# Kernel optimization log

Measured on AMD Instinct MI355X. Metric: run time of the kernel, lower is better.

## Reference

```python
import jax, jax.numpy as jnp
import numpy as np

NUM_HEADS = 4
GROUPS = 8
EPS = 1e-5


def group_norm(x, w, b):
    B, C, H, W, D = x.shape
    xg = x.reshape(B, GROUPS, C // GROUPS, H, W, D)
    mu = xg.mean(axis=(2, 3, 4, 5), keepdims=True)
    var = xg.var(axis=(2, 3, 4, 5), keepdims=True)
    xn = ((xg - mu) * jax.lax.rsqrt(var + EPS)).reshape(B, C, H, W, D)
    return xn * w[None, :, None, None, None] + b[None, :, None, None, None]


def avg_pool2x(t, H, W, D):
    # t: [N, d, H, W, D] -> [N, d, H/2, W/2, D/2] via 2x2x2 block mean
    N, d = t.shape[:2]
    t = t.reshape(N, d, H // 2, 2, W // 2, 2, D // 2, 2)
    return t.mean(axis=(3, 5, 7))


def setup_inputs() -> dict:
    key = jax.random.key(0)
    ks = jax.random.split(key, 4)
    B, C, H, W, D = 2, 128, 24, 24, 24
    x = jax.random.normal(ks[0], (B, C, H, W, D), dtype=jnp.float32)
    gn_w = jnp.ones((C,), jnp.float32)
    gn_b = jnp.zeros((C,), jnp.float32)
    qkv_w = jax.random.normal(ks[1], (3 * C, C), dtype=jnp.float32) * 0.02
    qkv_b = jnp.zeros((3 * C,), jnp.float32)
    proj_w = jax.random.normal(ks[2], (C, C), dtype=jnp.float32) * 0.02
    proj_b = jnp.zeros((C,), jnp.float32)
    return {"x": x, "gn_w": gn_w, "gn_b": gn_b, "qkv_w": qkv_w,
            "qkv_b": qkv_b, "proj_w": proj_w, "proj_b": proj_b}


def reference(x, gn_w, gn_b, qkv_w, qkv_b, proj_w, proj_b):
    B, C, H, W, D = x.shape
    hd = C // NUM_HEADS
    spatial = H * W * D
    residual = x

    xn = group_norm(x, gn_w, gn_b)
    # 1x1x1 conv == channel matmul
    qkv = jnp.einsum('oc,bchwd->bohwd', qkv_w, xn) + qkv_b[None, :, None, None, None]
    qkv = qkv.reshape(B, 3, NUM_HEADS, hd, spatial)
    q, k, v = qkv[:, 0], qkv[:, 1], qkv[:, 2]  # [B, h, d, N]

    if spatial > 1024:
        k3 = k.reshape(B * NUM_HEADS, hd, H, W, D)
        v3 = v.reshape(B * NUM_HEADS, hd, H, W, D)
        k = avg_pool2x(k3, H, W, D).reshape(B, NUM_HEADS, hd, -1)
        v = avg_pool2x(v3, H, W, D).reshape(B, NUM_HEADS, hd, -1)

    scale = hd ** -0.5
    attn = jnp.einsum('bhdn,bhdm->bhnm', q * scale, k)
    attn = jax.nn.softmax(attn, axis=-1)
    out = jnp.einsum('bhnm,bhdm->bhdn', attn, v)
    out = out.reshape(B, C, H, W, D)
    out = jnp.einsum('oc,bchwd->bohwd', proj_w, out) + proj_b[None, :, None, None, None]
    return out + residual
```

## Files before the change

### kernel.cpp

```cpp
#include <hip/hip_runtime.h>
#include <hip/hip_bf16.h>

#define SB 2
#define SC 128
#define SS 13824
#define SNH 4
#define SHD 32
#define SKV 1728
#define GN_N 221184.0f
#define QSCALE 0.25504771249f

typedef unsigned int uint;
typedef unsigned short ushort;
typedef __bf16 bf16x8 __attribute__((ext_vector_type(8)));
typedef float f32x16 __attribute__((ext_vector_type(16)));

__device__ inline ushort f2bf(float v){
  __hip_bfloat16 h = __float2bfloat16(v);
  return *reinterpret_cast<ushort*>(&h);
}
__device__ inline float bf2f(ushort u){
  union { ushort s[2]; float f; } x; x.s[0] = 0; x.s[1] = u; return x.f;
}
__device__ inline uint pk2(float a, float b){
  __hip_bfloat162 h = __float22bfloat162_rn(make_float2(a, b));
  return *reinterpret_cast<uint*>(&h);
}
__device__ inline bf16x8 ldg8(const ushort* p){
  union { uint4 q; bf16x8 b; } u;
  u.q = *reinterpret_cast<const uint4*>(p);
  return u.b;
}
__device__ inline f32x16 mfma32(bf16x8 a, bf16x8 b, f32x16 c){
  return __builtin_amdgcn_mfma_f32_32x32x16_bf16(a, b, c, 0, 0, 0);
}
__device__ inline int rowmap(int r, int hl){
  return (r & 3) + 8 * ((r >> 2) & 1) + 4 * hl + 16 * (r >> 3);
}
__device__ inline float vexp2(float x){
  float r;
  asm("v_exp_f32 %0, %1" : "=v"(r) : "v"(x));
  return r;
}

__global__ __launch_bounds__(256) void k_stats(const float* __restrict__ x, float* __restrict__ chsums){
  int bid = blockIdx.x;
  int b = bid >> 7, c = bid & 127;
  const float4* p = reinterpret_cast<const float4*>(x + (size_t)(b * 128 + c) * SS);
  float s = 0.f, q = 0.f;
  for (int i = threadIdx.x; i < SS / 4; i += 256){
    float4 v = p[i];
    s += v.x + v.y + v.z + v.w;
    q += v.x * v.x + v.y * v.y + v.z * v.z + v.w * v.w;
  }
  for (int off = 32; off; off >>= 1){ s += __shfl_down(s, off, 64); q += __shfl_down(q, off, 64); }
  __shared__ float ls[4][2];
  int w = threadIdx.x >> 6, lane = threadIdx.x & 63;
  if (lane == 0){ ls[w][0] = s; ls[w][1] = q; }
  __syncthreads();
  if (threadIdx.x == 0){
    float S = ls[0][0] + ls[1][0] + ls[2][0] + ls[3][0];
    float Q = ls[0][1] + ls[1][1] + ls[2][1] + ls[3][1];
    chsums[(b * 128 + c) * 2] = S;
    chsums[(b * 128 + c) * 2 + 1] = Q;
  }
}

__global__ __launch_bounds__(256) void k_params(const float* __restrict__ chsums,
                                                const float* __restrict__ gn_w, const float* __restrict__ gn_b,
                                                const float* __restrict__ qkv_w, const float* __restrict__ qkv_b,
                                                const float* __restrict__ proj_w,
                                                ushort* __restrict__ Wp, float* __restrict__ biasP,
                                                ushort* __restrict__ pw){
  int tid = blockIdx.x * 256 + threadIdx.x;
  if (tid < 768){
    int b = tid / 384, o = tid % 384;
    float mul = (o < 128) ? QSCALE : 1.0f;
    ushort* wrow = Wp + (size_t)(b * 384 + o) * 128;
    float acc = 0.f;
    for (int g = 0; g < 8; ++g){
      float S = 0.f, Q = 0.f;
      for (int ch = g * 16; ch < g * 16 + 16; ++ch){
        S += chsums[(b * 128 + ch) * 2];
        Q += chsums[(b * 128 + ch) * 2 + 1];
      }
      float mu = S * (1.0f / GN_N);
      float var = Q * (1.0f / GN_N) - mu * mu;
      float rs = rsqrtf(var + 1e-5f);
      for (int ci = 0; ci < 16; ++ci){
        int c = g * 16 + ci;
        float a = gn_w[c] * rs;
        float be = gn_b[c] - mu * a;
        float wv = qkv_w[o * 128 + c];
        acc += wv * be;
        wrow[c] = f2bf(wv * a * mul);
      }
    }
    biasP[b * 384 + o] = (qkv_b[o] + acc) * mul;
  } else if (tid < 896){
    int o = tid - 768;
    for (int c = 0; c < 128; ++c) pw[o * 128 + c] = f2bf(proj_w[o * 128 + c]);
  }
}

__global__ __launch_bounds__(128) void k_qkv(const float* __restrict__ x, const ushort* __restrict__ Wp,
                                             const float* __restrict__ biasP,
                                             ushort* __restrict__ Qt, ushort* __restrict__ KVt){
  int bid = blockIdx.x;
  int st2 = bid % 432;
  int b  = bid / 432;
  int t = threadIdx.x, w = t >> 6, lane = t & 63, hl = lane >> 5, ln = lane & 31;
  int s0 = st2 * 32;
  int s = s0 + ln;
  const float* xb = x + (size_t)b * 128 * SS;
  bf16x8 afr[8];
  #pragma unroll
  for (int ks = 0; ks < 8; ++ks){
    int cb = ks * 16 + hl * 8;
    float xv[8];
    #pragma unroll
    for (int j = 0; j < 8; ++j)
      xv[j] = xb[(size_t)(cb + j) * SS + s];
    union { uint u[4]; bf16x8 b8; } f;
    #pragma unroll
    for (int j2 = 0; j2 < 4; ++j2) f.u[j2] = pk2(xv[2 * j2], xv[2 * j2 + 1]);
    afr[ks] = f.b8;
  }
  for (int oi = 0; oi < 6; ++oi){
    int o0 = (w * 6 + oi) * 32;
    f32x16 acc = {};
    const ushort* wrow = Wp + (size_t)(b * 384 + o0 + ln) * 128 + hl * 8;
    #pragma unroll
    for (int ks = 0; ks < 8; ++ks)
      acc = mfma32(afr[ks], ldg8(wrow + ks * 16), acc);
    float bo = biasP[b * 384 + o0 + ln];
    if (o0 < 128){
      #pragma unroll
      for (int r = 0; r < 16; r += 2){
        int srow = s0 + rowmap(r, hl);
        uint pr = pk2(acc[r] + bo, acc[r + 1] + bo);
        Qt[(size_t)(b * SS + srow) * 128 + o0 + ln] = (ushort)pr;
        Qt[(size_t)(b * SS + srow + 1) * 128 + o0 + ln] = (ushort)(pr >> 16);
      }
    } else {
      #pragma unroll
      for (int r = 0; r < 16; r += 2){
        int srow = s0 + rowmap(r, hl);
        uint pr = pk2(acc[r] + bo, acc[r + 1] + bo);
        KVt[(size_t)(b * SS + srow) * 256 + (o0 - 128) + ln] = (ushort)pr;
        KVt[(size_t)(b * SS + srow + 1) * 256 + (o0 - 128) + ln] = (ushort)(pr >> 16);
      }
    }
  }
}

__global__ __launch_bounds__(256) void k_pool(const ushort* __restrict__ KVt,
                                              ushort* __restrict__ kfr, ushort* __restrict__ vfr){
  int bid = blockIdx.x;
  int mt = bid % 27;
  int h  = (bid / 27) & 3;
  int b  = bid / 108;
  int m0 = mt * 64;
  int t = threadIdx.x;
  int kl = t & 63, o = t >> 6;
  int m = m0 + kl;
  int h2 = m / 144; int rem = m - h2 * 144; int w2 = rem / 12; int d2 = rem - w2 * 12;
  int sb = h2 * 1152 + w2 * 48 + d2 * 2;
  const ushort* base = KVt + (size_t)b * SS * 256 + h * 32 + o * 8;
  float ks[8] = {0,0,0,0,0,0,0,0}, vs[8] = {0,0,0,0,0,0,0,0};
  #pragma unroll
  for (int i = 0; i < 2; ++i)
    #pragma unroll
    for (int jj = 0; jj < 2; ++jj)
      #pragma unroll
      for (int kk = 0; kk < 2; ++kk){
        const ushort* row = base + (size_t)(sb + i * 576 + jj * 24 + kk) * 256;
        union { uint4 q; ushort us[8]; } K8, V8;
        K8.q = *reinterpret_cast<const uint4*>(row);
        V8.q = *reinterpret_cast<const uint4*>(row + 128);
        #pragma unroll
        for (int j = 0; j < 8; ++j){ ks[j] += bf2f(K8.us[j]); vs[j] += bf2f(V8.us[j]); }
      }
  union { uint u[4]; uint4 q; } KW;
  #pragma unroll
  for (int j2 = 0; j2 < 4; ++j2)
    KW.u[j2] = pk2(ks[2 * j2] * 0.125f, ks[2 * j2 + 1] * 0.125f);
  int call = 2 * (kl >> 5) + (o >> 1);
  int lane = (kl & 31) + 32 * (o & 1);
  size_t kb_ = ((size_t)((b * 4 + h) * 27 + mt) * 4 + call) * 512 + lane * 8;
  *reinterpret_cast<uint4*>(&kfr[kb_]) = KW.q;
  __shared__ ushort V_lds[32][72];
  #pragma unroll
  for (int j2 = 0; j2 < 4; ++j2){
    uint pv = pk2(vs[2 * j2] * 0.125f, vs[2 * j2 + 1] * 0.125f);
    V_lds[o * 8 + 2 * j2][kl] = (ushort)pv;
    V_lds[o * 8 + 2 * j2 + 1][kl] = (ushort)(pv >> 16);
  }
  __syncthreads();
  int d = t & 31, ko = t >> 5;
  uint4 vv = *reinterpret_cast<const uint4*>(&V_lds[d][ko * 8]);
  int c = ko >> 1, hl2 = ko & 1;
  int lane2 = d + 32 * hl2;
  size_t vb_ = ((size_t)((b * 4 + h) * 27 + mt) * 4 + c) * 512 + lane2 * 8;
  *reinterpret_cast<uint4*>(&vfr[vb_]) = vv;
}

#define PVSTEP(Parr, i4, vf, oac)                                    \
  {                                                                  \
    uint a0 = Parr[(i4) + 0], a1 = Parr[(i4) + 1];                   \
    uint b0 = Parr[(i4) + 2], b1 = Parr[(i4) + 3];                   \
    asm("v_permlane32_swap_b32 %0, %1" : "+v"(a0), "+v"(b0));        \
    asm("v_permlane32_swap_b32 %0, %1" : "+v"(a1), "+v"(b1));        \
    union { uint u[4]; bf16x8 b8; } pf;                              \
    pf.u[0] = a0; pf.u[1] = a1; pf.u[2] = b0; pf.u[3] = b1;          \
    oac = mfma32(vf, pf.b8, oac);                                    \
    lacc = mfma32(ones, pf.b8, lacc);                                \
  }

__global__ __launch_bounds__(256, 2) void k_attn(const ushort* __restrict__ Qt, const ushort* __restrict__ kfr,
                                                 const ushort* __restrict__ vfr, const ushort* __restrict__ pw,
                                                 const float* __restrict__ pb, const float* __restrict__ xres,
                                                 float* __restrict__ out){
  int bid = blockIdx.x;
  int qt = bid % 432;
  int b  = bid / 432;
  int t = threadIdx.x, w = t >> 6, lane = t & 63, hl = lane >> 5, ln = lane & 31;
  int n = qt * 32 + ln;
  int h = w;
  int bh = b * 4 + h;
  const ushort* qrow = Qt + (size_t)(b * SS + n) * 128 + h * 32;
  bf16x8 qf0 = ldg8(qrow + hl * 8);
  bf16x8 qf1 = ldg8(qrow + 16 + hl * 8);
  const ushort* kbase = kfr + (size_t)bh * 27 * 2048 + (size_t)lane * 8;
  const ushort* vbase = vfr + (size_t)bh * 27 * 2048 + (size_t)lane * 8;
  union { ushort us[8]; bf16x8 b8; } one8;
  #pragma unroll
  for (int j = 0; j < 8; ++j) one8.us[j] = 0x3F80;
  bf16x8 ones = one8.b8;
  const f32x16 fz = {};
  f32x16 oA = fz, oB = fz, lacc = fz;
  bf16x8 kc0 = ldg8(kbase), kc1 = ldg8(kbase + 512);
  bf16x8 kc2 = ldg8(kbase + 1024), kc3 = ldg8(kbase + 1536);
  for (int it = 0; it < 27; ++it){
    const ushort* vp = vbase + it * 2048;
    bf16x8 v0 = ldg8(vp), v1 = ldg8(vp + 512), v2 = ldg8(vp + 1024), v3 = ldg8(vp + 1536);
    int itn = it + 1; if (itn == 27) itn = 0;
    const ushort* kpn = kbase + itn * 2048;
    bf16x8 kn0 = ldg8(kpn), kn1 = ldg8(kpn + 512);
    bf16x8 kn2 = ldg8(kpn + 1024), kn3 = ldg8(kpn + 1536);
    f32x16 s0 = mfma32(kc0, qf0, fz);
    s0 = mfma32(kc1, qf1, s0);
    f32x16 s1 = mfma32(kc2, qf0, fz);
    s1 = mfma32(kc3, qf1, s1);
    #pragma unroll
    for (int r = 0; r < 16; ++r) s0[r] = vexp2(s0[r]);
    #pragma unroll
    for (int r = 0; r < 16; ++r) s1[r] = vexp2(s1[r]);
    uint P0[8], P1[8];
    #pragma unroll
    for (int i = 0; i < 8; ++i) P0[i] = pk2(s0[2 * i], s0[2 * i + 1]);
    #pragma unroll
    for (int i = 0; i < 8; ++i) P1[i] = pk2(s1[2 * i], s1[2 * i + 1]);
    PVSTEP(P0, 0, v0, oA)
    PVSTEP(P0, 4, v1, oB)
    PVSTEP(P1, 0, v2, oA)
    PVSTEP(P1, 4, v3, oB)
    kc0 = kn0; kc1 = kn1; kc2 = kn2; kc3 = kn3;
  }
  float inv = 1.f / lacc[0];
  __shared__ ushort OT[32][136];
  #pragma unroll
  for (int r = 0; r < 16; r += 2){
    int d = rowmap(r, hl);
    uint pr = pk2((oA[r] + oB[r]) * inv, (oA[r + 1] + oB[r + 1]) * inv);
    *reinterpret_cast<uint*>(&OT[ln][h * 32 + d]) = pr;
  }
  __syncthreads();
  bf16x8 bfr[8];
  #pragma unroll
  for (int ks = 0; ks < 8; ++ks)
    bfr[ks] = ldg8(&OT[ln][ks * 16 + hl * 8]);
  f32x16 acc = fz;
  const ushort* arow = pw + (size_t)(w * 32 + ln) * 128 + hl * 8;
  #pragma unroll
  for (int ks = 0; ks < 8; ++ks)
    acc = mfma32(ldg8(arow + ks * 16), bfr[ks], acc);
  #pragma unroll
  for (int r = 0; r < 16; ++r){
    int o = w * 32 + rowmap(r, hl);
    size_t idx = (size_t)(b * 128 + o) * SS + n;
    out[idx] = acc[r] + pb[o] + xres[idx];
  }
}

extern "C" void kernel_launch(void* const* d_in, const int* in_sizes, int n_in,
                              void* d_out, int out_size, void* d_ws, size_t ws_size,
                              hipStream_t stream){
  const float* x      = (const float*)d_in[0];
  const float* gn_w   = (const float*)d_in[1];
  const float* gn_b   = (const float*)d_in[2];
  const float* qkv_w  = (const float*)d_in[3];
  const float* qkv_b  = (const float*)d_in[4];
  const float* proj_w = (const float*)d_in[5];
  const float* proj_b = (const float*)d_in[6];
  float* out = (float*)d_out;
  char* ws = (char*)d_ws;

  float*  chsums = (float*) (ws + 0);
  ushort* Wp     = (ushort*)(ws + 2048);
  float*  biasP  = (float*) (ws + 198656);
  ushort* pw     = (ushort*)(ws + 201728);
  ushort* Qt     = (ushort*)(ws + 234496);
  ushort* KVt    = (ushort*)(ws + 7312384);
  ushort* kfr    = (ushort*)(ws + 21468160);
  ushort* vfr    = (ushort*)(ws + 22352896);

  k_stats <<<256, 256, 0, stream>>>(x, chsums);
  k_params<<<4,   256, 0, stream>>>(chsums, gn_w, gn_b, qkv_w, qkv_b, proj_w, Wp, biasP, pw);
  k_qkv   <<<864, 128, 0, stream>>>(x, Wp, biasP, Qt, KVt);
  k_pool  <<<216, 256, 0, stream>>>(KVt, kfr, vfr);
  k_attn  <<<864, 256, 0, stream>>>(Qt, kfr, vfr, pw, proj_b, x, out);
}
```

Before: 95.37 us.

## Split QKV projection across two blocks and restructure pooling to process all heads per block

The QKV projection kernel now launches twice as many blocks, each computing half of the output channels for a 32-position tile. This gives more parallelism at the cost of loading and converting the x tile twice. The pooling kernel is rewritten so each block handles all four heads for 64 pooled positions. Each half-wave reads full contiguous 256-channel KV rows, a cross-half shuffle combines the results, and everything is staged in LDS before scattering into the fragment layouts. This improves coalescing, but the pooling grid drops to 54 blocks, which can leave much of the GPU idle.

```diff
diff --git a/kernel.cpp b/kernel.cpp
--- a/kernel.cpp
+++ b/kernel.cpp
@@ -107,8 +107,9 @@
                                              const float* __restrict__ biasP,
                                              ushort* __restrict__ Qt, ushort* __restrict__ KVt){
   int bid = blockIdx.x;
-  int st2 = bid % 432;
-  int b  = bid / 432;
+  int half = bid & 1;
+  int st2 = (bid >> 1) % 432;
+  int b  = bid / 864;
   int t = threadIdx.x, w = t >> 6, lane = t & 63, hl = lane >> 5, ln = lane & 31;
   int s0 = st2 * 32;
   int s = s0 + ln;
@@ -126,8 +127,9 @@
     for (int j2 = 0; j2 < 4; ++j2) f.u[j2] = pk2(xv[2 * j2], xv[2 * j2 + 1]);
     afr[ks] = f.b8;
   }
-  for (int oi = 0; oi < 6; ++oi){
-    int o0 = (w * 6 + oi) * 32;
+  int tb = half * 6 + w * 3;
+  for (int oi = 0; oi < 3; ++oi){
+    int o0 = (tb + oi) * 32;
     f32x16 acc = {};
     const ushort* wrow = Wp + (size_t)(b * 384 + o0 + ln) * 128 + hl * 8;
     #pragma unroll
@@ -158,51 +160,60 @@
                                               ushort* __restrict__ kfr, ushort* __restrict__ vfr){
   int bid = blockIdx.x;
   int mt = bid % 27;
-  int h  = (bid / 27) & 3;
-  int b  = bid / 108;
+  int b  = bid / 27;
   int m0 = mt * 64;
-  int t = threadIdx.x;
+  int t = threadIdx.x, w = t >> 6, lane = t & 63, hl = lane >> 5, ln = lane & 31;
+  __shared__ ushort K_lds[64][136];
+  __shared__ ushort V_lds[64][136];
+  const ushort* kvb = KVt + (size_t)b * SS * 256;
+  for (int mi = 0; mi < 16; ++mi){
+    int ml = w * 16 + mi;
+    int m = m0 + ml;
+    int h2 = m / 144; int rem = m - h2 * 144; int w2 = rem / 12; int d2 = rem - w2 * 12;
+    int sb = h2 * 1152 + w2 * 48 + d2 * 2 + hl;
+    float acc[8] = {0,0,0,0,0,0,0,0};
+    #pragma unroll
+    for (int i = 0; i < 2; ++i)
+      #pragma unroll
+      for (int jj = 0; jj < 2; ++jj){
+        const ushort* row = kvb + (size_t)(sb + i * 576 + jj * 24) * 256 + ln * 8;
+        union { uint4 q; ushort us[8]; } u;
+        u.q = *reinterpret_cast<const uint4*>(row);
+        #pragma unroll
+        for (int j = 0; j < 8; ++j) acc[j] += bf2f(u.us[j]);
+      }
+    #pragma unroll
+    for (int j = 0; j < 8; ++j) acc[j] += __shfl_xor(acc[j], 32, 64);
+    if (hl == 0){
+      union { uint u[4]; uint4 q; } pk;
+      #pragma unroll
+      for (int j2 = 0; j2 < 4; ++j2)
+        pk.u[j2] = pk2(acc[2 * j2] * 0.125f, acc[2 * j2 + 1] * 0.125f);
+      if (ln < 16) *reinterpret_cast<uint4*>(&K_lds[ml][ln * 8]) = pk.q;
+      else         *reinterpret_cast<uint4*>(&V_lds[ml][(ln - 16) * 8]) = pk.q;
+    }
+  }
+  __syncthreads();
   int kl = t & 63, o = t >> 6;
-  int m = m0 + kl;
-  int h2 = m / 144; int rem = m - h2 * 144; int w2 = rem / 12; int d2 = rem - w2 * 12;
-  int sb = h2 * 1152 + w2 * 48 + d2 * 2;
-  const ushort* base = KVt + (size_t)b * SS * 256 + h * 32 + o * 8;
-  float ks[8] = {0,0,0,0,0,0,0,0}, vs[8] = {0,0,0,0,0,0,0,0};
-  #pragma unroll
-  for (int i = 0; i < 2; ++i)
-    #pragma unroll
-    for (int jj = 0; jj < 2; ++jj)
-      #pragma unroll
-      for (int kk = 0; kk < 2; ++kk){
-        const ushort* row = base + (size_t)(sb + i * 576 + jj * 24 + kk) * 256;
-        union { uint4 q; ushort us[8]; } K8, V8;
-        K8.q = *reinterpret_cast<const uint4*>(row);
-        V8.q = *reinterpret_cast<const uint4*>(row + 128);
-        #pragma unroll
-        for (int j = 0; j < 8; ++j){ ks[j] += bf2f(K8.us[j]); vs[j] += bf2f(V8.us[j]); }
-      }
-  union { uint u[4]; uint4 q; } KW;
-  #pragma unroll
-  for (int j2 = 0; j2 < 4; ++j2)
-    KW.u[j2] = pk2(ks[2 * j2] * 0.125f, ks[2 * j2 + 1] * 0.125f);
-  int call = 2 * (kl >> 5) + (o >> 1);
-  int lane = (kl & 31) + 32 * (o & 1);
-  size_t kb_ = ((size_t)((b * 4 + h) * 27 + mt) * 4 + call) * 512 + lane * 8;
-  *reinterpret_cast<uint4*>(&kfr[kb_]) = KW.q;
-  __shared__ ushort V_lds[32][72];
-  #pragma unroll
-  for (int j2 = 0; j2 < 4; ++j2){
-    uint pv = pk2(vs[2 * j2] * 0.125f, vs[2 * j2 + 1] * 0.125f);
-    V_lds[o * 8 + 2 * j2][kl] = (ushort)pv;
-    V_lds[o * 8 + 2 * j2 + 1][kl] = (ushort)(pv >> 16);
-  }
-  __syncthreads();
+  #pragma unroll
+  for (int h = 0; h < 4; ++h){
+    uint4 kk_ = *reinterpret_cast<const uint4*>(&K_lds[kl][h * 32 + o * 8]);
+    int call = 2 * (kl >> 5) + (o >> 1);
+    int lane2 = (kl & 31) + 32 * (o & 1);
+    size_t kb_ = ((size_t)((b * 4 + h) * 27 + mt) * 4 + call) * 512 + lane2 * 8;
+    *reinterpret_cast<uint4*>(&kfr[kb_]) = kk_;
+  }
   int d = t & 31, ko = t >> 5;
-  uint4 vv = *reinterpret_cast<const uint4*>(&V_lds[d][ko * 8]);
   int c = ko >> 1, hl2 = ko & 1;
-  int lane2 = d + 32 * hl2;
-  size_t vb_ = ((size_t)((b * 4 + h) * 27 + mt) * 4 + c) * 512 + lane2 * 8;
-  *reinterpret_cast<uint4*>(&vfr[vb_]) = vv;
+  #pragma unroll
+  for (int h = 0; h < 4; ++h){
+    union { ushort us[8]; uint4 q; } vv;
+    #pragma unroll
+    for (int j = 0; j < 8; ++j)
+      vv.us[j] = V_lds[c * 16 + hl2 * 8 + j][h * 32 + d];
+    size_t vb_ = ((size_t)((b * 4 + h) * 27 + mt) * 4 + c) * 512 + (d + 32 * hl2) * 8;
+    *reinterpret_cast<uint4*>(&vfr[vb_]) = vv.q;
+  }
 }
 
 #define PVSTEP(Parr, i4, vf, oac)                                    \
@@ -315,9 +326,9 @@
   ushort* kfr    = (ushort*)(ws + 21468160);
   ushort* vfr    = (ushort*)(ws + 22352896);
 
-  k_stats <<<256, 256, 0, stream>>>(x, chsums);
-  k_params<<<4,   256, 0, stream>>>(chsums, gn_w, gn_b, qkv_w, qkv_b, proj_w, Wp, biasP, pw);
-  k_qkv   <<<864, 128, 0, stream>>>(x, Wp, biasP, Qt, KVt);
-  k_pool  <<<216, 256, 0, stream>>>(KVt, kfr, vfr);
-  k_attn  <<<864, 256, 0, stream>>>(Qt, kfr, vfr, pw, proj_b, x, out);
-}
+  k_stats <<<256,  256, 0, stream>>>(x, chsums);
+  k_params<<<4,    256, 0, stream>>>(chsums, gn_w, gn_b, qkv_w, qkv_b, proj_w, Wp, biasP, pw);
+  k_qkv   <<<1728, 128, 0, stream>>>(x, Wp, biasP, Qt, KVt);
+  k_pool  <<<54,   256, 0, stream>>>(KVt, kfr, vfr);
+  k_attn  <<<864,  256, 0, stream>>>(Qt, kfr, vfr, pw, proj_b, x, out);
+}
```

Measured after the change: 102.8 us. 1.08x slower.
